# Kernel optimization log

Hardware: AMD Instinct MI355X
Metric: run time of the kernel (lower is better)

## Reference

```python
import jax, jax.numpy as jnp
import numpy as np

EMBED_DIM = 1024
N1 = 4096
N2 = 4096


def setup_inputs() -> dict:
    key = jax.random.key(0)
    ks = jax.random.split(key, 14)
    s = 1.0 / np.sqrt(EMBED_DIM)
    def lin(k):
        kw, kb = jax.random.split(k)
        W = jax.random.uniform(kw, (EMBED_DIM, EMBED_DIM), jnp.float32, -s, s)
        b = jax.random.uniform(kb, (EMBED_DIM,), jnp.float32, -s, s)
        return W, b
    Wq1, bq1 = lin(ks[0]); Wk1, bk1 = lin(ks[1]); Wv1, bv1 = lin(ks[2])
    Wq2, bq2 = lin(ks[3]); Wk2, bk2 = lin(ks[4]); Wv2, bv2 = lin(ks[5])
    x1 = jax.random.normal(ks[6], (N1, EMBED_DIM), jnp.float32)
    x2 = jax.random.normal(ks[7], (N2, EMBED_DIM), jnp.float32)
    return {
        "input_tensor1": x1, "input_tensor2": x2,
        "Wq1": Wq1, "bq1": bq1, "Wk1": Wk1, "bk1": bk1, "Wv1": Wv1, "bv1": bv1,
        "Wq2": Wq2, "bq2": bq2, "Wk2": Wk2, "bk2": bk2, "Wv2": Wv2, "bv2": bv2,
    }


def reference(input_tensor1, input_tensor2,
              Wq1, bq1, Wk1, bk1, Wv1, bv1,
              Wq2, bq2, Wk2, bk2, Wv2, bv2):
    scale = 1.0 / jnp.sqrt(jnp.asarray(EMBED_DIM, input_tensor1.dtype))
    # torch Linear: y = x @ W.T + b
    q1 = input_tensor1 @ Wq1.T + bq1   # [N1, D]
    k1 = input_tensor1 @ Wk1.T + bk1
    v1 = input_tensor1 @ Wv1.T + bv1
    q2 = input_tensor2 @ Wq2.T + bq2   # [N2, D]
    k2 = input_tensor2 @ Wk2.T + bk2
    v2 = input_tensor2 @ Wv2.T + bv2
    # stream-2 queries attend over stream-1 keys/values
    scores1 = (q2 @ k1.T) * scale                  # [N2, N1]
    probs1 = jax.nn.softmax(scores1, axis=-1)      # dropout p=0 -> identity
    context1 = probs1 @ v1                         # [N2, D]
    # stream-1 queries attend over stream-2 keys/values
    scores2 = (q1 @ k2.T) * scale                  # [N1, N2]
    probs2 = jax.nn.softmax(scores2, axis=-1)
    context2 = probs2 @ v2                         # [N1, D]
    return (context1, context2)
```

## Files before the change

### kernel.cpp

```cpp
#include <hip/hip_runtime.h>
#include <hip/hip_bf16.h>
#include <cstdint>
#include <cstddef>

#define DEVINL __device__ __forceinline__

typedef __attribute__((ext_vector_type(4))) float   f32x4;
typedef __bf16 bf16x8 __attribute__((ext_vector_type(8)));
typedef __attribute__((ext_vector_type(4))) short   short4v;
typedef __attribute__((ext_vector_type(4))) float   float4v;

static constexpr int DIM = 1024;
static constexpr int NTOK = 4096;

DEVINL unsigned short f2bf(float f) {
  unsigned u = __float_as_uint(f);
  u += 0x7FFF + ((u >> 16) & 1);
  return (unsigned short)(u >> 16);
}
DEVINL float bf2f(unsigned short s) {
  return __uint_as_float(((unsigned)s) << 16);
}

DEVINL void gll16(const void* g, void* l) {
  __builtin_amdgcn_global_load_lds(
      (const __attribute__((address_space(1))) void*)g,
      (__attribute__((address_space(3))) void*)l, 16, 0, 0);
}

struct B3 { int bx, by, bz; };
DEVINL B3 xcd_remap(int GX, int GY, int GZ) {
  const int flat = blockIdx.x + GX * (blockIdx.y + GY * blockIdx.z);
  const int nwg  = GX * GY * GZ;
  const int chunk = nwg >> 3;
  const int vbid = (flat & 7) * chunk + (flat >> 3);
  B3 r;
  r.bx = vbid % GX;
  r.by = (vbid / GX) % GY;
  r.bz = vbid / (GX * GY);
  return r;
}

DEVINL void core256v2(const unsigned short* __restrict__ A, int lda,
                      const unsigned short* __restrict__ B, int ldb,
                      int K, int brow, int bcol, f32x4 acc[8][4])
{
  __shared__ unsigned short lds[65536];
  const int t = threadIdx.x;
  const int w = t >> 6, l = t & 63;
  const int wr = w >> 2, wc = w & 3;
  const int srow = l >> 3;
  const int scol = ((l & 7) ^ srow) << 3;
  const int l15 = l & 15;
  const int cs0 = (((l >> 4) << 3)        ^ ((l & 7) << 3));
  const int cs1 = ((32 + ((l >> 4) << 3)) ^ ((l & 7) << 3));

  const unsigned short* aL = A + (size_t)(brow * 256 + srow) * lda + scol;
  const unsigned short* bL = B + (size_t)(bcol * 256 + srow) * ldb + scol;

#pragma unroll
  for (int m = 0; m < 8; ++m)
#pragma unroll
    for (int n = 0; n < 4; ++n) {
      f32x4 z = {0.f, 0.f, 0.f, 0.f};
      acc[m][n] = z;
    }

#define STA_(Sbase, h, r, kt)                                                  \
  gll16(aL + (size_t)((r)*128 + (h)*64 + (w << 3)) * lda + (size_t)(kt)*64,    \
        lds + (Sbase) + ((r)*128 + (h)*64 + (w << 3)) * 64)
#define STB_(Sbase, h, r, kt)                                                  \
  { const int g16_ = w + (r)*8;                                                \
    const int r0_ = (g16_ >> 2)*64 + (h)*32 + (g16_ & 3)*8;                    \
    gll16(bL + (size_t)r0_ * ldb + (size_t)(kt)*64, lds + (Sbase) + r0_ * 64); }
#define LDA_(Abase, mh)                                                        \
  _Pragma("unroll")                                                            \
  for (int m4 = 0; m4 < 4; ++m4) {                                             \
    const unsigned short* p_ = lds + (Abase) + (wr*128 + (mh)*64 + m4*16 + l15)*64; \
    af[m4][0] = *(const bf16x8*)(p_ + cs0);                                    \
    af[m4][1] = *(const bf16x8*)(p_ + cs1);                                    \
  }
#define LDB_(Bbase, nh)                                                        \
  _Pragma("unroll")                                                            \
  for (int n2 = 0; n2 < 2; ++n2) {                                             \
    const unsigned short* p_ = lds + (Bbase) + (wc*64 + (nh)*32 + n2*16 + l15)*64;  \
    bfr[n2][0] = *(const bf16x8*)(p_ + cs0);                                   \
    bfr[n2][1] = *(const bf16x8*)(p_ + cs1);                                   \
  }
#define MF_(mh, nh)                                                            \
  __builtin_amdgcn_s_setprio(1);                                               \
  _Pragma("unroll")                                                            \
  for (int m4 = 0; m4 < 4; ++m4)                                               \
  _Pragma("unroll")                                                            \
  for (int n2 = 0; n2 < 2; ++n2) {                                             \
    f32x4 c_ = acc[(mh)*4 + m4][(nh)*2 + n2];                                  \
    c_ = __builtin_amdgcn_mfma_f32_16x16x32_bf16(af[m4][0], bfr[n2][0], c_, 0,0,0); \
    c_ = __builtin_amdgcn_mfma_f32_16x16x32_bf16(af[m4][1], bfr[n2][1], c_, 0,0,0); \
    acc[(mh)*4 + m4][(nh)*2 + n2] = c_;                                        \
  }                                                                            \
  __builtin_amdgcn_s_setprio(0);
#define VMW4() asm volatile("s_waitcnt vmcnt(4)" ::: "memory")
#define VMW0() asm volatile("s_waitcnt vmcnt(0)" ::: "memory")
#define BARR() do { asm volatile("" ::: "memory");                             \
                    __builtin_amdgcn_s_barrier();                              \
                    asm volatile("" ::: "memory"); } while (0)

  STA_(0, 0, 0, 0); STA_(0, 0, 1, 0); STB_(16384, 0, 0, 0); STB_(16384, 0, 1, 0);
  STA_(0, 1, 0, 0); STA_(0, 1, 1, 0); STB_(16384, 1, 0, 0); STB_(16384, 1, 1, 0);

  bf16x8 af[4][2], bfr[2][2];
  const int NT = K >> 6;
  for (int kt = 0; kt < NT - 1; ++kt) {
    const int Ab = (kt & 1) * 32768;
    const int Bb = Ab + 16384;
    const int Sa = ((kt & 1) ^ 1) * 32768;
    const int Sb = Sa + 16384;

    VMW4(); BARR();
    STA_(Sa, 0, 0, kt + 1); STA_(Sa, 0, 1, kt + 1);
    STB_(Sb, 0, 0, kt + 1); STB_(Sb, 0, 1, kt + 1);
    LDA_(Ab, 0); LDB_(Bb, 0);
    MF_(0, 0);

    VMW4(); BARR();
    STA_(Sa, 1, 0, kt + 1); STA_(Sa, 1, 1, kt + 1);
    STB_(Sb, 1, 0, kt + 1); STB_(Sb, 1, 1, kt + 1);
    LDA_(Ab, 1);
    MF_(1, 0);

    LDB_(Bb, 1);
    MF_(1, 1);

    LDA_(Ab, 0);
    MF_(0, 1);
  }

  {
    const int kt = NT - 1;
    const int Ab = (kt & 1) * 32768;
    const int Bb = Ab + 16384;
    VMW4(); BARR();
    LDA_(Ab, 0); LDB_(Bb, 0);
    MF_(0, 0);
    VMW0(); BARR();
    LDA_(Ab, 1);
    MF_(1, 0);
    LDB_(Bb, 1);
    MF_(1, 1);
    LDA_(Ab, 0);
    MF_(0, 1);
  }
#undef STA_
#undef STB_
#undef LDA_
#undef LDB_
#undef MF_
#undef VMW4
#undef VMW0
#undef BARR
}

DEVINL void core256x128(const unsigned short* __restrict__ A, int lda,
                        const unsigned short* __restrict__ B, int ldb,
                        int K, int brow, int bcol, f32x4 acc[4][4])
{
  __shared__ unsigned short lds[73728];
  const int t = threadIdx.x;
  const int w = t >> 6, l = t & 63;
  const int wr = w >> 1, wc = w & 1;
  const int l15 = l & 15;
  const int scol = ((l & 3) ^ ((l >> 3) & 3)) << 3;
  const int cs   = (((l >> 4) ^ ((l15 >> 1) & 3)) << 3);

  const unsigned short* aL = A + (size_t)(brow * 256 + w * 16 + (l >> 2)) * lda + scol;
  const unsigned short* bL = B + (size_t)(bcol * 128 + w * 16 + (l >> 2)) * ldb + scol;

#pragma unroll
  for (int m = 0; m < 4; ++m)
#pragma unroll
    for (int n = 0; n < 4; ++n) {
      f32x4 z = {0.f, 0.f, 0.f, 0.f};
      acc[m][n] = z;
    }

#define STAGE(buf, kt)                                                         \
  {                                                                            \
    gll16(aL + (size_t)(kt) * 32,                                              \
          lds + (buf) * 12288 + w * 512);                                      \
    gll16(aL + (size_t)128 * lda + (size_t)(kt) * 32,                          \
          lds + (buf) * 12288 + 4096 + w * 512);                               \
    gll16(bL + (size_t)(kt) * 32,                                              \
          lds + (buf) * 12288 + 8192 + w * 512);                               \
  }

  const int NT = K >> 5;

  STAGE(0, 0); STAGE(1, 1); STAGE(2, 2); STAGE(3, 3);

  bf16x8 af[4], bfv[4];
  int cur = 0;
  for (int kt = 0; kt < NT; ++kt) {
    int st = cur + 4; if (st >= 6) st -= 6;
    if (kt + 4 < NT) STAGE(st, kt + 4);

    const int rem = NT - 1 - kt;
    if (rem >= 4)      asm volatile("s_waitcnt vmcnt(12)" ::: "memory");
    else if (rem == 3) asm volatile("s_waitcnt vmcnt(9)"  ::: "memory");
    else if (rem == 2) asm volatile("s_waitcnt vmcnt(6)"  ::: "memory");
    else if (rem == 1) asm volatile("s_waitcnt vmcnt(3)"  ::: "memory");
    else               asm volatile("s_waitcnt vmcnt(0)"  ::: "memory");
    asm volatile("" ::: "memory");
    __builtin_amdgcn_s_barrier();
    asm volatile("" ::: "memory");

    const unsigned short* base = lds + cur * 12288;
#pragma unroll
    for (int m = 0; m < 4; ++m)
      af[m] = *(const bf16x8*)(base + (wr * 64 + m * 16 + l15) * 32 + cs);
#pragma unroll
    for (int n = 0; n < 4; ++n)
      bfv[n] = *(const bf16x8*)(base + 8192 + (wc * 64 + n * 16 + l15) * 32 + cs);

    __builtin_amdgcn_s_setprio(1);
#pragma unroll
    for (int m = 0; m < 4; ++m)
#pragma unroll
      for (int n = 0; n < 4; ++n)
        acc[m][n] = __builtin_amdgcn_mfma_f32_16x16x32_bf16(af[m], bfv[n], acc[m][n], 0, 0, 0);
    __builtin_amdgcn_s_setprio(0);

    cur = (cur + 1 == 6) ? 0 : cur + 1;
  }
#undef STAGE
}

__global__ __launch_bounds__(512, 1)
void gemm256_scores(const unsigned short* __restrict__ A,
                    const unsigned short* __restrict__ B,
                    unsigned short* __restrict__ S, float scale)
{
  const B3 b = xcd_remap(16, 16, 1);
  f32x4 acc[8][4];
  core256v2(A, DIM, B, DIM, DIM, b.by, b.bx, acc);

  const int t = threadIdx.x, w = t >> 6, l = t & 63;
  const int wr = w >> 2, wc = w & 3;
  const int r4 = (l >> 4) * 4, c = l & 15;
  const int row0 = b.by * 256 + wr * 128;
  const int col0 = b.bx * 256 + wc * 64;
#pragma unroll
  for (int mf = 0; mf < 8; ++mf)
#pragma unroll
    for (int nf = 0; nf < 4; ++nf)
#pragma unroll
      for (int i = 0; i < 4; ++i)
        S[(size_t)(row0 + mf*16 + r4 + i) * NTOK + col0 + nf*16 + c] =
            f2bf(acc[mf][nf][i] * scale);
}

__global__ __launch_bounds__(512, 1)
void qkv256(const unsigned short* __restrict__ x1, const unsigned short* __restrict__ x2,
            const unsigned short* __restrict__ W6,
            const float* bq1, const float* bk1, const float* bv1,
            const float* bq2, const float* bk2, const float* bv2,
            unsigned short* q1, unsigned short* k1, unsigned short* v1T,
            unsigned short* q2, unsigned short* k2, unsigned short* v2T)
{
  const B3 b = xcd_remap(4, 16, 6);
  const int g = b.bz;
  const unsigned short* A = (g < 3) ? x1 : x2;
  const unsigned short* W = W6 + (size_t)g * (DIM * DIM);
  const float* bias = (g == 0) ? bq1 : (g == 1) ? bk1 : (g == 2) ? bv1
                    : (g == 3) ? bq2 : (g == 4) ? bk2 : bv2;
  unsigned short* out = (g == 0) ? q1 : (g == 1) ? k1 : (g == 2) ? v1T
                      : (g == 3) ? q2 : (g == 4) ? k2 : v2T;
  const bool vT = (g == 2 || g == 5);

  f32x4 acc[8][4];
  core256v2(A, DIM, W, DIM, DIM, b.by, b.bx, acc);

  const int t = threadIdx.x, w = t >> 6, l = t & 63;
  const int wr = w >> 2, wc = w & 3;
  const int r4 = (l >> 4) * 4, c = l & 15;
  const int row0 = b.by * 256 + wr * 128;
  const int col0 = b.bx * 256 + wc * 64;

  float bias_v[4];
#pragma unroll
  for (int nf = 0; nf < 4; ++nf) bias_v[nf] = bias[col0 + nf*16 + c];

  if (!vT) {
#pragma unroll
    for (int mf = 0; mf < 8; ++mf)
#pragma unroll
      for (int nf = 0; nf < 4; ++nf)
#pragma unroll
        for (int i = 0; i < 4; ++i)
          out[(size_t)(row0 + mf*16 + r4 + i) * DIM + col0 + nf*16 + c] =
              f2bf(acc[mf][nf][i] + bias_v[nf]);
  } else {
#pragma unroll
    for (int mf = 0; mf < 8; ++mf)
#pragma unroll
      for (int nf = 0; nf < 4; ++nf) {
        short4v pk;
#pragma unroll
        for (int i = 0; i < 4; ++i) pk[i] = (short)f2bf(acc[mf][nf][i] + bias_v[nf]);
        *(short4v*)(out + (size_t)(col0 + nf*16 + c) * NTOK + row0 + mf*16 + r4) = pk;
      }
  }
}

__global__ __launch_bounds__(512, 2)
void pv_gemm(const unsigned short* __restrict__ S1,
             const unsigned short* __restrict__ S2,
             const unsigned short* __restrict__ vTcat,
             float* __restrict__ out)
{
  const B3 b = xcd_remap(16, 16, 1);
  const int bx = b.bx, by = b.by;
  const unsigned short* A = (bx < 8) ? S1 : S2;

  f32x4 acc[4][4];
  core256x128(A, NTOK, vTcat, NTOK, NTOK, by, bx, acc);

  const int t = threadIdx.x, w = t >> 6, l = t & 63;
  const int wr = w >> 1, wc = w & 1;
  const int rr = (l >> 4) * 4, cc = l & 15;
#pragma unroll
  for (int m = 0; m < 4; ++m) {
    const int row0 = by * 256 + wr * 64 + m * 16 + rr;
#pragma unroll
    for (int n = 0; n < 4; ++n) {
      const int cg = bx * 128 + wc * 64 + n * 16 + cc;
      float* dstBase = (cg < 1024) ? (out + cg) : (out + 4194304 + (cg - 1024));
#pragma unroll
      for (int i = 0; i < 4; ++i)
        dstBase[(size_t)(row0 + i) * 1024] = acc[m][n][i];
    }
  }
}

__global__ __launch_bounds__(256)
void softmax_inplace(unsigned short* __restrict__ S)
{
  const int row = blockIdx.x;
  unsigned short* r = S + (size_t)row * NTOK;
  const int t = threadIdx.x, wave = t >> 6, lane = t & 63;
  __shared__ float red[4];

  bf16x8 d0 = *(const bf16x8*)(r + t * 8);
  bf16x8 d1 = *(const bf16x8*)(r + 2048 + t * 8);
  float v[16];
  {
    const unsigned short* p0 = (const unsigned short*)&d0;
    const unsigned short* p1 = (const unsigned short*)&d1;
#pragma unroll
    for (int j = 0; j < 8; ++j) { v[j] = bf2f(p0[j]); v[8 + j] = bf2f(p1[j]); }
  }
  float mx = v[0];
#pragma unroll
  for (int j = 1; j < 16; ++j) mx = fmaxf(mx, v[j]);
#pragma unroll
  for (int o = 32; o > 0; o >>= 1) mx = fmaxf(mx, __shfl_xor(mx, o));
  if (lane == 0) red[wave] = mx;
  __syncthreads();
  mx = fmaxf(fmaxf(red[0], red[1]), fmaxf(red[2], red[3]));

  float s = 0.f;
#pragma unroll
  for (int j = 0; j < 16; ++j) { v[j] = __expf(v[j] - mx); s += v[j]; }
#pragma unroll
  for (int o = 32; o > 0; o >>= 1) s += __shfl_xor(s, o);
  __syncthreads();
  if (lane == 0) red[wave] = s;
  __syncthreads();
  s = red[0] + red[1] + red[2] + red[3];
  const float inv = 1.0f / s;

  unsigned short o0[8], o1[8];
#pragma unroll
  for (int j = 0; j < 8; ++j) { o0[j] = f2bf(v[j] * inv); o1[j] = f2bf(v[8 + j] * inv); }
  *(bf16x8*)(r + t * 8)        = *(const bf16x8*)o0;
  *(bf16x8*)(r + 2048 + t * 8) = *(const bf16x8*)o1;
}

__global__ __launch_bounds__(256)
void cvt2(const float* __restrict__ a, const float* __restrict__ b,
          unsigned short* __restrict__ oa, unsigned short* __restrict__ ob)
{
  const float* in = blockIdx.y ? b : a;
  unsigned short* out = blockIdx.y ? ob : oa;
  const size_t i = ((size_t)blockIdx.x * 256 + threadIdx.x) * 4;
  float4v x = *(const float4v*)(in + i);
  short4v o;
#pragma unroll
  for (int j = 0; j < 4; ++j) o[j] = (short)f2bf(x[j]);
  *(short4v*)(out + i) = o;
}

__global__ __launch_bounds__(256)
void cvt_w(const float* w0, const float* w1, const float* w2,
           const float* w3, const float* w4, const float* w5,
           unsigned short* __restrict__ W6)
{
  const float* srcs[6] = {w0, w1, w2, w3, w4, w5};
  const float* in = srcs[blockIdx.y];
  unsigned short* out = W6 + (size_t)blockIdx.y * (DIM * DIM);
  const size_t i = ((size_t)blockIdx.x * 256 + threadIdx.x) * 4;
  float4v x = *(const float4v*)(in + i);
  short4v o;
#pragma unroll
  for (int j = 0; j < 4; ++j) o[j] = (short)f2bf(x[j]);
  *(short4v*)(out + i) = o;
}

extern "C" void kernel_launch(void* const* d_in, const int* in_sizes, int n_in,
                              void* d_out, int out_size, void* d_ws, size_t ws_size,
                              hipStream_t stream)
{
  const float* x1  = (const float*)d_in[0];
  const float* x2  = (const float*)d_in[1];
  const float* Wq1 = (const float*)d_in[2];  const float* bq1 = (const float*)d_in[3];
  const float* Wk1 = (const float*)d_in[4];  const float* bk1 = (const float*)d_in[5];
  const float* Wv1 = (const float*)d_in[6];  const float* bv1 = (const float*)d_in[7];
  const float* Wq2 = (const float*)d_in[8];  const float* bq2 = (const float*)d_in[9];
  const float* Wk2 = (const float*)d_in[10]; const float* bk2 = (const float*)d_in[11];
  const float* Wv2 = (const float*)d_in[12]; const float* bv2 = (const float*)d_in[13];
  float* out = (float*)d_out;

  unsigned short* ws  = (unsigned short*)d_ws;
  const size_t NTD = (size_t)NTOK * DIM;
  const size_t SM  = (size_t)NTOK * NTOK;
  unsigned short* x1b = ws;
  unsigned short* x2b = x1b + NTD;
  unsigned short* W6  = x2b + NTD;
  unsigned short* S1  = ws;
  unsigned short* S2  = ws + SM;
  unsigned short* q1  = ws + 2 * SM;
  unsigned short* k1  = q1 + NTD;
  unsigned short* q2  = k1 + NTD;
  unsigned short* k2  = q2 + NTD;
  unsigned short* vT  = k2 + NTD;
  unsigned short* v1T = vT;
  unsigned short* v2T = vT + NTD;

  const dim3 blk(256);
  cvt2 <<<dim3(NTD / 1024, 2), blk, 0, stream>>>(x1, x2, x1b, x2b);
  cvt_w<<<dim3((DIM * DIM) / 1024, 6), blk, 0, stream>>>(Wq1, Wk1, Wv1, Wq2, Wk2, Wv2, W6);

  qkv256<<<dim3(4, 16, 6), dim3(512), 0, stream>>>(
      x1b, x2b, W6, bq1, bk1, bv1, bq2, bk2, bv2, q1, k1, v1T, q2, k2, v2T);

  const float scale = 0.03125f;

  gemm256_scores<<<dim3(16, 16), dim3(512), 0, stream>>>(q2, k1, S1, scale);
  gemm256_scores<<<dim3(16, 16), dim3(512), 0, stream>>>(q1, k2, S2, scale);
  softmax_inplace<<<dim3(2 * NTOK), blk, 0, stream>>>(S1);

  pv_gemm<<<dim3(16, 16), dim3(512), 0, stream>>>(S1, S2, vT, out);
}
```

Baseline: 244.8 us.

## Simplify GEMM pipeline to full-tile prefetch with one barrier per K-step

```diff
diff --git a/kernel.cpp b/kernel.cpp
--- a/kernel.cpp
+++ b/kernel.cpp
@@ -41,7 +41,7 @@
   return r;
 }
 
-DEVINL void core256v2(const unsigned short* __restrict__ A, int lda,
+DEVINL void core256v3(const unsigned short* __restrict__ A, int lda,
                       const unsigned short* __restrict__ B, int ldb,
                       int K, int brow, int bcol, f32x4 acc[8][4])
 {
@@ -73,6 +73,11 @@
   { const int g16_ = w + (r)*8;                                                \
     const int r0_ = (g16_ >> 2)*64 + (h)*32 + (g16_ & 3)*8;                    \
     gll16(bL + (size_t)r0_ * ldb + (size_t)(kt)*64, lds + (Sbase) + r0_ * 64); }
+#define STAGE8(base, kt)                                                       \
+  STA_((base), 0, 0, kt); STA_((base), 0, 1, kt);                              \
+  STB_((base) + 16384, 0, 0, kt); STB_((base) + 16384, 0, 1, kt);              \
+  STA_((base), 1, 0, kt); STA_((base), 1, 1, kt);                              \
+  STB_((base) + 16384, 1, 0, kt); STB_((base) + 16384, 1, 1, kt);
 #define LDA_(Abase, mh)                                                        \
   _Pragma("unroll")                                                            \
   for (int m4 = 0; m4 < 4; ++m4) {                                             \
@@ -99,63 +104,39 @@
     acc[(mh)*4 + m4][(nh)*2 + n2] = c_;                                        \
   }                                                                            \
   __builtin_amdgcn_s_setprio(0);
-#define VMW4() asm volatile("s_waitcnt vmcnt(4)" ::: "memory")
 #define VMW0() asm volatile("s_waitcnt vmcnt(0)" ::: "memory")
 #define BARR() do { asm volatile("" ::: "memory");                             \
                     __builtin_amdgcn_s_barrier();                              \
                     asm volatile("" ::: "memory"); } while (0)
 
-  STA_(0, 0, 0, 0); STA_(0, 0, 1, 0); STB_(16384, 0, 0, 0); STB_(16384, 0, 1, 0);
-  STA_(0, 1, 0, 0); STA_(0, 1, 1, 0); STB_(16384, 1, 0, 0); STB_(16384, 1, 1, 0);
+  STAGE8(0, 0);
+  VMW0(); BARR();
 
   bf16x8 af[4][2], bfr[2][2];
   const int NT = K >> 6;
-  for (int kt = 0; kt < NT - 1; ++kt) {
-    const int Ab = (kt & 1) * 32768;
-    const int Bb = Ab + 16384;
-    const int Sa = ((kt & 1) ^ 1) * 32768;
-    const int Sb = Sa + 16384;
-
-    VMW4(); BARR();
-    STA_(Sa, 0, 0, kt + 1); STA_(Sa, 0, 1, kt + 1);
-    STB_(Sb, 0, 0, kt + 1); STB_(Sb, 0, 1, kt + 1);
-    LDA_(Ab, 0); LDB_(Bb, 0);
+  for (int kt = 0; kt < NT; ++kt) {
+    const int cur = (kt & 1) * 32768;
+    const int oth = cur ^ 32768;
+
+    if (kt + 1 < NT) { STAGE8(oth, kt + 1); }
+
+    LDA_(cur, 0); LDB_(cur + 16384, 0);
     MF_(0, 0);
-
-    VMW4(); BARR();
-    STA_(Sa, 1, 0, kt + 1); STA_(Sa, 1, 1, kt + 1);
-    STB_(Sb, 1, 0, kt + 1); STB_(Sb, 1, 1, kt + 1);
-    LDA_(Ab, 1);
+    LDA_(cur, 1);
     MF_(1, 0);
-
-    LDB_(Bb, 1);
+    LDB_(cur + 16384, 1);
     MF_(1, 1);
-
-    LDA_(Ab, 0);
+    LDA_(cur, 0);
     MF_(0, 1);
-  }
-
-  {
-    const int kt = NT - 1;
-    const int Ab = (kt & 1) * 32768;
-    const int Bb = Ab + 16384;
-    VMW4(); BARR();
-    LDA_(Ab, 0); LDB_(Bb, 0);
-    MF_(0, 0);
+
     VMW0(); BARR();
-    LDA_(Ab, 1);
-    MF_(1, 0);
-    LDB_(Bb, 1);
-    MF_(1, 1);
-    LDA_(Ab, 0);
-    MF_(0, 1);
   }
 #undef STA_
 #undef STB_
+#undef STAGE8
 #undef LDA_
 #undef LDB_
 #undef MF_
-#undef VMW4
 #undef VMW0
 #undef BARR
 }
@@ -241,7 +222,7 @@
 {
   const B3 b = xcd_remap(16, 16, 1);
   f32x4 acc[8][4];
-  core256v2(A, DIM, B, DIM, DIM, b.by, b.bx, acc);
+  core256v3(A, DIM, B, DIM, DIM, b.by, b.bx, acc);
 
   const int t = threadIdx.x, w = t >> 6, l = t & 63;
   const int wr = w >> 2, wc = w & 3;
@@ -277,7 +258,7 @@
   const bool vT = (g == 2 || g == 5);
 
   f32x4 acc[8][4];
-  core256v2(A, DIM, W, DIM, DIM, b.by, b.bx, acc);
+  core256v3(A, DIM, W, DIM, DIM, b.by, b.bx, acc);
 
   const int t = threadIdx.x, w = t >> 6, l = t & 63;
   const int wr = w >> 2, wc = w & 3;
```

New measurement: 248.7 us. No clear change (+1.6%).
